# Kernel optimization log

Measured on AMD Instinct MI355X. Metric: run time of the kernel, lower is better.

## Reference

```python
import jax, jax.numpy as jnp
import numpy as np


def _conv(x, kernel):
    # x: [N, C, H, W], kernel: [O, I, kh, kw]; torch conv2d padding=1 (symmetric both dims)
    return jax.lax.conv_general_dilated(
        x, kernel, window_strides=(1, 1), padding=((1, 1), (1, 1)),
        dimension_numbers=("NCHW", "OIHW", "NCHW"))


def setup_inputs() -> dict:
    key = jax.random.key(0)
    k1, k2 = jax.random.split(key)
    shape = (2, 7, 7, 3, 256, 256)  # bs, ah, aw, c, h, w
    infer = jax.random.normal(k1, shape, dtype=jnp.float32)
    ref = jax.random.normal(k2, shape, dtype=jnp.float32)
    return {"infer": infer, "ref": ref}


def reference(infer, ref):
    bs, ah, aw, c, h, w = infer.shape
    x = infer.reshape(bs * ah * aw, c, h, w)
    y = ref.reshape(bs * ah * aw, c, h, w)
    # fixed gradient kernels, identical across all 3x3 in/out channel pairs
    kh = jnp.broadcast_to(
        jnp.array([-0.5, 0.0, 0.5], jnp.float32).reshape(1, 1, 1, 3), (3, 3, 1, 3))
    kv = jnp.broadcast_to(
        jnp.array([-0.5, 0.0, 0.5], jnp.float32).reshape(1, 1, 3, 1), (3, 3, 3, 1))
    # torch padding=1 on a (1,3) kernel -> output (h+2, w); on (3,1) -> (h, w+2)
    loss_h = jnp.mean(jnp.abs(_conv(x, kh) - _conv(y, kh)))
    loss_v = jnp.mean(jnp.abs(_conv(x, kv) - _conv(y, kv)))
    return (loss_h + loss_v) / 2.0
```

## Files before the change

kernel.cpp:

```cpp
#include <hip/hip_runtime.h>


#define W 256
#define NIMG 98
#define CH_STRIDE 65536
#define TH 8
#define NSTRIP 32
#define NBLK (NIMG * NSTRIP)
#define SCALE (0.25f / 6472704.0f)

struct Row6 { float4 a0, a1, a2, b0, b1, b2; };

__device__ __forceinline__ int clampg(int g) {
  return g < 0 ? 0 : (g > 255 ? 255 : g);
}

__device__ __forceinline__ Row6 issue_row(const float* __restrict__ xb,
                                          const float* __restrict__ yb,
                                          int g) {
  const int ro = g * W;
  Row6 r;
  r.a0 = *(const float4*)(xb + ro);
  r.a1 = *(const float4*)(xb + ro + CH_STRIDE);
  r.a2 = *(const float4*)(xb + ro + 2 * CH_STRIDE);
  r.b0 = *(const float4*)(yb + ro);
  r.b1 = *(const float4*)(yb + ro + CH_STRIDE);
  r.b2 = *(const float4*)(yb + ro + 2 * CH_STRIDE);
  return r;
}

__device__ __forceinline__ float4 combine(const Row6& r, float m) {
  float4 d;
  d.x = m * ((r.a0.x - r.b0.x) + (r.a1.x - r.b1.x) + (r.a2.x - r.b2.x));
  d.y = m * ((r.a0.y - r.b0.y) + (r.a1.y - r.b1.y) + (r.a2.y - r.b2.y));
  d.z = m * ((r.a0.z - r.b0.z) + (r.a1.z - r.b1.z) + (r.a2.z - r.b2.z));
  d.w = m * ((r.a0.w - r.b0.w) + (r.a1.w - r.b1.w) + (r.a2.w - r.b2.w));
  return d;
}

__device__ __forceinline__ float band_body(const float* __restrict__ x,
                                           const float* __restrict__ y) {
  const int lane  = threadIdx.x;
  const int b     = blockIdx.x;
  const int n     = b >> 5;
  const int strip = b & 31;
  const int r0    = strip * TH;

  const float* xb = x + (size_t)n * 3 * CH_STRIDE + (lane << 2);
  const float* yb = y + (size_t)n * 3 * CH_STRIDE + (lane << 2);

  Row6 s0 = issue_row(xb, yb, clampg(r0 - 1));
  Row6 s1 = issue_row(xb, yb, r0);
  Row6 pend = issue_row(xb, yb, r0 + 1);

  float4 dprev = combine(s0, (r0 - 1 >= 0) ? 1.f : 0.f);
  float4 dcur  = combine(s1, 1.f);

  float acc = 0.f;
  #pragma unroll
  for (int r = 0; r < TH; ++r) {
    Row6 nxt = issue_row(xb, yb, clampg(r0 + r + 2));
    float4 dnext = combine(pend, (r0 + r + 1 <= 255) ? 1.f : 0.f);

    float lm = __shfl_up(dcur.w, 1);
    if (lane == 0) lm = 0.f;
    float rp = __shfl_down(dcur.x, 1);
    if (lane == 63) rp = 0.f;
    acc += fabsf(dcur.y - lm) + fabsf(dcur.z - dcur.x)
         + fabsf(dcur.w - dcur.y) + fabsf(rp - dcur.z);

    acc += fabsf(dnext.x - dprev.x) + fabsf(dnext.y - dprev.y)
         + fabsf(dnext.z - dprev.z) + fabsf(dnext.w - dprev.w);

    dprev = dcur; dcur = dnext; pend = nxt;
  }

  #pragma unroll
  for (int off = 32; off > 0; off >>= 1)
    acc += __shfl_down(acc, off, 64);
  return acc;
}

__global__ __launch_bounds__(64) void detail_stage1(
    const float* __restrict__ x, const float* __restrict__ y,
    float* __restrict__ partial) {
  float s = band_body(x, y);
  if (threadIdx.x == 0) partial[blockIdx.x] = s;
}

__global__ __launch_bounds__(64) void detail_stage1_atomic(
    const float* __restrict__ x, const float* __restrict__ y,
    float* __restrict__ out) {
  float s = band_body(x, y);
  if (threadIdx.x == 0) atomicAdd(out, s * SCALE);
}

__global__ __launch_bounds__(256) void detail_stage2(
    const float* __restrict__ partial, float* __restrict__ out) {
  float acc = 0.f;
  for (int i = threadIdx.x; i < NBLK; i += 256) acc += partial[i];
  #pragma unroll
  for (int off = 32; off > 0; off >>= 1)
    acc += __shfl_down(acc, off, 64);
  __shared__ float ws[4];
  if ((threadIdx.x & 63) == 0) ws[threadIdx.x >> 6] = acc;
  __syncthreads();
  if (threadIdx.x == 0) out[0] = (ws[0] + ws[1] + ws[2] + ws[3]) * SCALE;
}

extern "C" void kernel_launch(void* const* d_in, const int* in_sizes, int n_in,
                              void* d_out, int out_size, void* d_ws, size_t ws_size,
                              hipStream_t stream) {
  const float* infer = (const float*)d_in[0];
  const float* ref   = (const float*)d_in[1];
  float* out = (float*)d_out;

  if (ws_size >= NBLK * sizeof(float)) {
    float* partial = (float*)d_ws;
    detail_stage1<<<NBLK, 64, 0, stream>>>(infer, ref, partial);
    detail_stage2<<<1, 256, 0, stream>>>(partial, out);
  } else {
    hipMemsetAsync(out, 0, sizeof(float), stream);
    detail_stage1_atomic<<<NBLK, 64, 0, stream>>>(infer, ref, out);
  }
}
```

Measured before the change: 171.5 us.

## Assign one output row per wave with XCD-swizzled 256-thread blocks

Replaces the per-wave 8-row strip loop with one row per wave: each wave loads the three neighbouring rows (above, current, below) for both inputs. Four waves are grouped into a 256-thread block, and block ids are remapped so consecutive tasks land on the same XCD. The goal is more parallelism and memory-level concurrency, plus better L2 locality for the row loads that neighbouring waves share. The cost is that each row is read three times from the cache hierarchy instead of once per strip, and there are more blocks, so the stage2 reduction has more partials to sum.

```diff
diff --git a/kernel.cpp b/kernel.cpp
--- a/kernel.cpp
+++ b/kernel.cpp
@@ -4,21 +4,16 @@
 #define W 256
 #define NIMG 98
 #define CH_STRIDE 65536
-#define TH 8
-#define NSTRIP 32
-#define NBLK (NIMG * NSTRIP)
+#define WAVES_PER_BLK 4
+#define NROWS (NIMG * 256)
+#define NBLK (NROWS / WAVES_PER_BLK)
+#define NXCD 8
 #define SCALE (0.25f / 6472704.0f)
 
 struct Row6 { float4 a0, a1, a2, b0, b1, b2; };
 
-__device__ __forceinline__ int clampg(int g) {
-  return g < 0 ? 0 : (g > 255 ? 255 : g);
-}
-
-__device__ __forceinline__ Row6 issue_row(const float* __restrict__ xb,
-                                          const float* __restrict__ yb,
-                                          int g) {
-  const int ro = g * W;
+__device__ __forceinline__ Row6 issue6(const float* __restrict__ xb,
+                                       const float* __restrict__ yb, int ro) {
   Row6 r;
   r.a0 = *(const float4*)(xb + ro);
   r.a1 = *(const float4*)(xb + ro + CH_STRIDE);
@@ -38,42 +33,35 @@
   return d;
 }
 
-__device__ __forceinline__ float band_body(const float* __restrict__ x,
-                                           const float* __restrict__ y) {
-  const int lane  = threadIdx.x;
-  const int b     = blockIdx.x;
-  const int n     = b >> 5;
-  const int strip = b & 31;
-  const int r0    = strip * TH;
+__device__ __forceinline__ float row_task(const float* __restrict__ x,
+                                          const float* __restrict__ y,
+                                          int task, int lane) {
+  const int n = task >> 8;
+  const int h = task & 255;
 
   const float* xb = x + (size_t)n * 3 * CH_STRIDE + (lane << 2);
   const float* yb = y + (size_t)n * 3 * CH_STRIDE + (lane << 2);
 
-  Row6 s0 = issue_row(xb, yb, clampg(r0 - 1));
-  Row6 s1 = issue_row(xb, yb, r0);
-  Row6 pend = issue_row(xb, yb, r0 + 1);
+  const int hm = (h > 0)   ? h - 1 : 0;
+  const int hp = (h < 255) ? h + 1 : 255;
 
-  float4 dprev = combine(s0, (r0 - 1 >= 0) ? 1.f : 0.f);
-  float4 dcur  = combine(s1, 1.f);
+  Row6 rm = issue6(xb, yb, hm * W);
+  Row6 rc = issue6(xb, yb, h  * W);
+  Row6 rp = issue6(xb, yb, hp * W);
 
-  float acc = 0.f;
-  #pragma unroll
-  for (int r = 0; r < TH; ++r) {
-    Row6 nxt = issue_row(xb, yb, clampg(r0 + r + 2));
-    float4 dnext = combine(pend, (r0 + r + 1 <= 255) ? 1.f : 0.f);
+  float4 dm = combine(rm, (h > 0)   ? 1.f : 0.f);
+  float4 dc = combine(rc, 1.f);
+  float4 dp = combine(rp, (h < 255) ? 1.f : 0.f);
 
-    float lm = __shfl_up(dcur.w, 1);
-    if (lane == 0) lm = 0.f;
-    float rp = __shfl_down(dcur.x, 1);
-    if (lane == 63) rp = 0.f;
-    acc += fabsf(dcur.y - lm) + fabsf(dcur.z - dcur.x)
-         + fabsf(dcur.w - dcur.y) + fabsf(rp - dcur.z);
+  float lm = __shfl_up(dc.w, 1);
+  if (lane == 0) lm = 0.f;
+  float rr = __shfl_down(dc.x, 1);
+  if (lane == 63) rr = 0.f;
+  float acc = fabsf(dc.y - lm) + fabsf(dc.z - dc.x)
+            + fabsf(dc.w - dc.y) + fabsf(rr - dc.z);
 
-    acc += fabsf(dnext.x - dprev.x) + fabsf(dnext.y - dprev.y)
-         + fabsf(dnext.z - dprev.z) + fabsf(dnext.w - dprev.w);
-
-    dprev = dcur; dcur = dnext; pend = nxt;
-  }
+  acc += fabsf(dp.x - dm.x) + fabsf(dp.y - dm.y)
+       + fabsf(dp.z - dm.z) + fabsf(dp.w - dm.w);
 
   #pragma unroll
   for (int off = 32; off > 0; off >>= 1)
@@ -81,17 +69,37 @@
   return acc;
 }
 
-__global__ __launch_bounds__(64) void detail_stage1(
+__device__ __forceinline__ int swz_block(int bid) {
+  const int chunk = NBLK / NXCD;
+  return (bid % NXCD) * chunk + bid / NXCD;
+}
+
+__device__ __forceinline__ float block_body(const float* __restrict__ x,
+                                            const float* __restrict__ y) {
+  const int tid  = threadIdx.x;
+  const int lane = tid & 63;
+  const int wv   = tid >> 6;
+  const int task = swz_block(blockIdx.x) * WAVES_PER_BLK + wv;
+
+  float s = row_task(x, y, task, lane);
+
+  __shared__ float ws[WAVES_PER_BLK];
+  if (lane == 0) ws[wv] = s;
+  __syncthreads();
+  return ws[0] + ws[1] + ws[2] + ws[3];
+}
+
+__global__ __launch_bounds__(256) void detail_stage1(
     const float* __restrict__ x, const float* __restrict__ y,
     float* __restrict__ partial) {
-  float s = band_body(x, y);
+  float s = block_body(x, y);
   if (threadIdx.x == 0) partial[blockIdx.x] = s;
 }
 
-__global__ __launch_bounds__(64) void detail_stage1_atomic(
+__global__ __launch_bounds__(256) void detail_stage1_atomic(
     const float* __restrict__ x, const float* __restrict__ y,
     float* __restrict__ out) {
-  float s = band_body(x, y);
+  float s = block_body(x, y);
   if (threadIdx.x == 0) atomicAdd(out, s * SCALE);
 }
 
@@ -117,10 +125,10 @@
 
   if (ws_size >= NBLK * sizeof(float)) {
     float* partial = (float*)d_ws;
-    detail_stage1<<<NBLK, 64, 0, stream>>>(infer, ref, partial);
+    detail_stage1<<<NBLK, 256, 0, stream>>>(infer, ref, partial);
     detail_stage2<<<1, 256, 0, stream>>>(partial, out);
   } else {
     hipMemsetAsync(out, 0, sizeof(float), stream);
-    detail_stage1_atomic<<<NBLK, 64, 0, stream>>>(infer, ref, out);
+    detail_stage1_atomic<<<NBLK, 256, 0, stream>>>(infer, ref, out);
   }
 }
```

Measured after the change: 180.5 us. +5.2%, slower.
